# Kernel optimization log

Hardware: AMD Instinct MI355X
Metric: run time of the kernel (lower is better)

## Reference

```python
import math
import jax, jax.numpy as jnp
import numpy as np

H = 12
D = 64  # head dim

def _heads(x):
    # [b, n, h*d] -> [b, h, n, d]
    b, n, _ = x.shape
    return x.reshape(b, n, H, D).transpose(0, 2, 1, 3)

def setup_inputs() -> dict:
    key = jax.random.key(0)
    ks = jax.random.split(key, 9)
    hs = 768
    s = 1.0 / math.sqrt(hs)
    return {
        "query_states": jax.random.normal(ks[0], (8, 1024, hs), jnp.float32),
        "key_states": jax.random.normal(ks[1], (8, 1024, hs), jnp.float32),
        "Wd": jax.random.normal(ks[2], (hs, hs), jnp.float32) * s,
        "Wq": jax.random.normal(ks[3], (hs, hs), jnp.float32) * s,
        "bq": jax.random.normal(ks[4], (hs,), jnp.float32) * 0.01,
        "Wk": jax.random.normal(ks[5], (hs, hs), jnp.float32) * s,
        "bk": jax.random.normal(ks[6], (hs,), jnp.float32) * 0.01,
        "Wv": jax.random.normal(ks[7], (hs, hs), jnp.float32) * s,
        "bv": jax.random.normal(ks[8], (hs,), jnp.float32) * 0.01,
    }

def reference(query_states, key_states, Wd, Wq, bq, Wk, bk, Wv, bv):
    # projections (torch Linear: x @ W.T + b)
    qd = _heads(query_states @ Wd.T)          # [b,h,n,d]
    kd = _heads(key_states @ Wd.T)
    q = _heads(query_states @ Wq.T + bq)
    k = _heads(key_states @ Wk.T + bk)
    v = _heads(key_states @ Wv.T + bv)
    # -0.5 * cdist(qd, kd)^2 = -0.5*(|qd|^2 + |kd|^2) + qd@kd^T
    qd_sq = jnp.sum(qd * qd, axis=-1)          # [b,h,n]
    kd_sq = jnp.sum(kd * kd, axis=-1)          # [b,h,m]
    quad = (qd @ jnp.swapaxes(kd, -1, -2)
            - 0.5 * qd_sq[..., :, None]
            - 0.5 * kd_sq[..., None, :])       # [b,h,n,m]
    lin = q @ jnp.swapaxes(k, -1, -2)          # [b,h,n,m]
    scores = (quad + lin) / math.sqrt(D)
    probs = jax.nn.softmax(scores, axis=-1)
    ctx = probs @ v                            # [b,h,n,d]
    b, _, n, _ = ctx.shape
    return ctx.transpose(0, 2, 1, 3).reshape(b, n, H * D)
```

## Files before the change

kernel.cpp:

```cpp
#include <hip/hip_runtime.h>
#include <stdint.h>

typedef __attribute__((ext_vector_type(8))) short short8;
typedef __attribute__((ext_vector_type(4))) short short4v;
typedef __attribute__((ext_vector_type(4))) float f32x4;
typedef __attribute__((ext_vector_type(16))) float f32x16;
typedef __attribute__((ext_vector_type(4))) int int4v;

static __device__ __forceinline__ unsigned short f2b(float f) {
  unsigned int u = __builtin_bit_cast(unsigned int, f);
  u += 0x7fffu + ((u >> 16) & 1u);
  return (unsigned short)(u >> 16);
}
static __device__ __forceinline__ float b2f(unsigned short b) {
  unsigned int u = ((unsigned int)b) << 16;
  return __builtin_bit_cast(float, u);
}

#define GLD16(gp, lp)                                                          \
  __builtin_amdgcn_global_load_lds(                                            \
      (const __attribute__((address_space(1))) void*)(gp),                     \
      (__attribute__((address_space(3))) void*)(lp), 16, 0, 0)

#define MFMA16 __builtin_amdgcn_mfma_f32_16x16x32_bf16
#define MFMA32 __builtin_amdgcn_mfma_f32_32x32x16_bf16

#define CVTPK(dst, lo, hi)                                                     \
  asm("v_cvt_pk_bf16_f32 %0, %1, %2" : "=v"(dst) : "v"(lo), "v"(hi))
#define PLSWAP(x, y)                                                           \
  asm volatile("v_permlane32_swap_b32 %0, %1" : "+v"(x), "+v"(y))

#define QSC 0.18033688011112113f
#define C2 0.09016844005556057f

__global__ void cvtx_kernel(const float* __restrict__ q,
                            const float* __restrict__ k,
                            unsigned short* __restrict__ Xq,
                            unsigned short* __restrict__ Xk) {
  const int bx = blockIdx.x;
  const bool lo = bx < 6144;
  const float* src = lo ? q : k;
  unsigned short* dst = lo ? Xq : Xk;
  const int i = (lo ? bx : bx - 6144) * 256 + threadIdx.x;
  float4 v = reinterpret_cast<const float4*>(src)[i];
  short4v o;
  o.x = (short)f2b(v.x);
  o.y = (short)f2b(v.y);
  o.z = (short)f2b(v.z);
  o.w = (short)f2b(v.w);
  reinterpret_cast<short4v*>(dst)[i] = o;
}

__global__ void cvtw_kernel(const float* __restrict__ Wd,
                            const float* __restrict__ Wq,
                            const float* __restrict__ Wk,
                            const float* __restrict__ Wv,
                            unsigned short* __restrict__ Wcq,
                            unsigned short* __restrict__ Wck) {
  const int bx = blockIdx.x;
  const int seg = bx / 576;
  const int i = (bx - seg * 576) * 256 + threadIdx.x;
  const float* src;
  unsigned short* dst;
  switch (seg) {
    case 0: src = Wd; dst = Wcq; break;
    case 1: src = Wq; dst = Wcq + 589824; break;
    case 2: src = Wd; dst = Wck; break;
    case 3: src = Wk; dst = Wck + 589824; break;
    default: src = Wv; dst = Wck + 1179648; break;
  }
  float4 v = reinterpret_cast<const float4*>(src)[i];
  short4v o;
  o.x = (short)f2b(v.x);
  o.y = (short)f2b(v.y);
  o.z = (short)f2b(v.z);
  o.w = (short)f2b(v.w);
  reinterpret_cast<short4v*>(dst)[i] = o;
}

__global__ __launch_bounds__(512, 2) void proj_kernel(
    const unsigned short* __restrict__ Xq, const unsigned short* __restrict__ Xk,
    const unsigned short* __restrict__ Wcq, const unsigned short* __restrict__ Wck,
    const float* __restrict__ bq, const float* __restrict__ bk,
    const float* __restrict__ bv, unsigned short* __restrict__ Qc,
    unsigned short* __restrict__ Kc, unsigned short* __restrict__ Vt) {
  __shared__ __align__(16) short lds[3][2][256 * 32];
  const int by = blockIdx.y;
  const bool mode0 = (by < 6);
  const unsigned short* X = mode0 ? Xq : Xk;
  const unsigned short* W = mode0 ? Wcq : Wck;
  const int col0 = (mode0 ? by : by - 6) * 256;
  const int row0 = blockIdx.x * 256;
  const int tid = threadIdx.x;
  const int lane = tid & 63;
  const int wid = tid >> 6;
  const int wm = wid >> 2;
  const int wn = wid & 3;
  const int l15 = lane & 15, l4 = lane >> 4;
  const int RSWZ = (l4 ^ ((l15 >> 1) & 3)) << 4;

  f32x4 acc[8][4];
#pragma unroll
  for (int i = 0; i < 8; ++i)
#pragma unroll
    for (int j = 0; j < 4; ++j) acc[i][j] = (f32x4){0.f, 0.f, 0.f, 0.f};

  auto stage = [&](int bufi, int k0) {
#pragma unroll
    for (int iss = 0; iss < 2; ++iss) {
      const int c = iss * 512 + tid;
      const int r = c >> 2;
      const int sl = (c & 3) ^ ((c >> 3) & 3);
      const unsigned short* gp = X + (size_t)(row0 + r) * 768 + k0 + sl * 8;
      GLD16(gp, (char*)&lds[bufi][0][0] + (size_t)c * 16);
    }
#pragma unroll
    for (int iss = 0; iss < 2; ++iss) {
      const int c = iss * 512 + tid;
      const int r = c >> 2;
      const int sl = (c & 3) ^ ((c >> 3) & 3);
      const unsigned short* gp = W + (size_t)(col0 + r) * 768 + k0 + sl * 8;
      GLD16(gp, (char*)&lds[bufi][1][0] + (size_t)c * 16);
    }
  };

  stage(0, 0);
  stage(1, 32);

#pragma unroll 3
  for (int kt = 0; kt < 24; ++kt) {
    if (kt < 23) {
      asm volatile("s_waitcnt vmcnt(4) lgkmcnt(0)" ::: "memory");
    } else {
      asm volatile("s_waitcnt vmcnt(0) lgkmcnt(0)" ::: "memory");
    }
    __builtin_amdgcn_s_barrier();
    asm volatile("" ::: "memory");
    if (kt < 22) stage((kt + 2) % 3, (kt + 2) * 32);

    const char* Ab = (const char*)&lds[kt % 3][0][0];
    const char* Bb = (const char*)&lds[kt % 3][1][0];
    short8 a[8], b[4];
#pragma unroll
    for (int mt = 0; mt < 8; ++mt) {
      const int r = wm * 128 + mt * 16 + l15;
      a[mt] = *reinterpret_cast<const short8*>(Ab + r * 64 + RSWZ);
    }
#pragma unroll
    for (int nt = 0; nt < 4; ++nt) {
      const int r = wn * 64 + nt * 16 + l15;
      b[nt] = *reinterpret_cast<const short8*>(Bb + r * 64 + RSWZ);
    }
#pragma unroll
    for (int mt = 0; mt < 8; ++mt)
#pragma unroll
      for (int nt = 0; nt < 4; ++nt)
        acc[mt][nt] = MFMA16(a[mt], b[nt], acc[mt][nt], 0, 0, 0);
  }

  const int mat = mode0 ? (col0 >= 768 ? 1 : 0) : ((by - 6) / 3);
  const int cbase = col0 - mat * 768 + wn * 64;
  const float* barr = mode0 ? bq : (mat == 2 ? bv : bk);
  if (!mode0 && mat == 2) {
#pragma unroll
    for (int nt = 0; nt < 4; ++nt) {
      const int cc = cbase + nt * 16 + l15;
      const int hh = cc >> 6, dd = cc & 63;
      const float bias = barr[cc];
#pragma unroll
      for (int mt = 0; mt < 8; ++mt) {
        const int row = row0 + wm * 128 + mt * 16 + l4 * 4;
        const int bb = row >> 10, nn = row & 1023;
        short4v pv;
#pragma unroll
        for (int i = 0; i < 4; ++i)
          pv[i] = (short)f2b(acc[mt][nt][i] + bias);
        *reinterpret_cast<short4v*>(
            Vt + ((size_t)(bb * 12 + hh) * 64 + dd) * 1024 + nn) = pv;
      }
    }
  } else {
    const float scale = mode0 ? QSC : 1.0f;
    unsigned short* outC = mode0 ? Qc : Kc;
#pragma unroll
    for (int nt = 0; nt < 4; ++nt) {
      const int cc = cbase + nt * 16 + l15;
      const int hh = cc >> 6, dd = cc & 63;
      const float bias = (mat >= 1) ? barr[cc] : 0.f;
#pragma unroll
      for (int mt = 0; mt < 8; ++mt) {
#pragma unroll
        for (int i = 0; i < 4; ++i) {
          const int row = row0 + wm * 128 + mt * 16 + l4 * 4 + i;
          const int bb = row >> 10, nn = row & 1023;
          outC[((size_t)(bb * 12 + hh) * 1024 + nn) * 128 + mat * 64 + dd] =
              f2b((acc[mt][nt][i] + bias) * scale);
        }
      }
    }
  }
}

__global__ __launch_bounds__(256) void wv_kernel(
    const unsigned short* __restrict__ Kc, unsigned short* __restrict__ wq,
    const unsigned short* __restrict__ Vt, unsigned short* __restrict__ Vs) {
  __shared__ float wf[1024];
  const int bh = blockIdx.x;
  const int t = threadIdx.x;
  const int part = t & 3;
  const unsigned short* Kb = Kc + (size_t)bh * 1024 * 128;
#pragma unroll
  for (int it = 0; it < 16; ++it) {
    const int key = it * 64 + (t >> 2);
    const short8* p =
        reinterpret_cast<const short8*>(Kb + (size_t)key * 128 + part * 16);
    float s = 0.f;
    short8 x0 = p[0], x1 = p[1];
#pragma unroll
    for (int j = 0; j < 8; ++j) {
      const float f0 = b2f((unsigned short)x0[j]);
      const float f1 = b2f((unsigned short)x1[j]);
      s += f0 * f0 + f1 * f1;
    }
    s += __shfl_xor(s, 1);
    s += __shfl_xor(s, 2);
    if (part == 0) {
      const unsigned short wb = f2b(__builtin_amdgcn_exp2f(-s * C2));
      wf[key] = b2f(wb);
      wq[(size_t)bh * 1024 + key] = wb;
    }
  }
  __syncthreads();
  const unsigned short* Vb = Vt + (size_t)bh * 64 * 1024;
  unsigned short* Ob = Vs + (size_t)bh * 64 * 1024;
#pragma unroll
  for (int i = 0; i < 32; ++i) {
    const int e0 = (i * 256 + t) * 8;
    const int k0 = e0 & 1023;
    short8 v = *reinterpret_cast<const short8*>(Vb + e0);
#pragma unroll
    for (int j = 0; j < 8; ++j)
      v[j] = (short)f2b(b2f((unsigned short)v[j]) * wf[k0 + j]);
    *reinterpret_cast<short8*>(Ob + e0) = v;
  }
}

__global__ __launch_bounds__(256, 3) void attn_kernel(
    const unsigned short* __restrict__ Qc, const unsigned short* __restrict__ Kc,
    const unsigned short* __restrict__ Vs, const unsigned short* __restrict__ wq,
    float* __restrict__ out) {
  __shared__ __align__(16) short kbuf[2][64 * 128];
  __shared__ __align__(16) short vbuf[2][64 * 64];
  __shared__ __align__(16) short wbuf[1024];

  const int bh = blockIdx.x % 96;
  const int qb = blockIdx.x / 96;
  const int b = bh / 12, h = bh - b * 12;
  const int lane = threadIdx.x & 63;
  const int w = threadIdx.x >> 6;
  const int l31 = lane & 31, l5 = lane >> 5;

  const unsigned short* Kg = Kc + (size_t)bh * 1024 * 128;
  const unsigned short* Vg = Vs + (size_t)bh * 64 * 1024;

  auto stageK = [&](int bufi, int kb) {
#pragma unroll
    for (int i = 0; i < 4; ++i) {
      const int slot = i * 256 + threadIdx.x;
      const int row = slot >> 4;
      const int d0 = ((slot & 15) ^ (row & 15)) * 8;
      const unsigned short* gp = Kg + (size_t)(kb * 64 + row) * 128 + d0;
      GLD16(gp, (char*)(&kbuf[bufi][0]) + (i * 256 + w * 64) * 16);
    }
  };
  auto stageV = [&](int bufi, int kb) {
#pragma unroll
    for (int i = 0; i < 2; ++i) {
      const int slot = i * 256 + threadIdx.x;
      const int row = slot >> 3;
      const int k0 = ((slot & 7) ^ (row & 7)) * 8;
      const unsigned short* gp = Vg + (size_t)row * 1024 + kb * 64 + k0;
      GLD16(gp, (char*)(&vbuf[bufi][0]) + (i * 256 + w * 64) * 16);
    }
  };

  stageK(0, 0);
  stageV(0, 0);
  if (w < 2) {
    const unsigned short* gp = wq + (size_t)bh * 1024 + (w * 64 + lane) * 8;
    GLD16(gp, (char*)(&wbuf[0]) + w * 1024);
  }

  const unsigned short* Qb =
      Qc + ((size_t)bh * 1024 + qb * 128 + w * 32 + l31) * 128 + l5 * 8;
  short8 qf[8];
#pragma unroll
  for (int s = 0; s < 8; ++s)
    qf[s] = *reinterpret_cast<const short8*>(Qb + s * 16);

  f32x16 o0, o1, la;
#pragma unroll
  for (int r = 0; r < 16; ++r) {
    o0[r] = 0.f;
    o1[r] = 0.f;
    la[r] = 0.f;
  }
  float m = -1e30f;

  const int S4 = (lane & 15) << 4;
  const int S3 = (lane & 7) << 4;
  const int ko = l5 * 16;

  asm volatile("s_waitcnt vmcnt(0)" ::: "memory");
  __syncthreads();

  int buf = 0;
  for (int kb = 0; kb < 16; ++kb) {
    if (kb < 15) {
      stageK(buf ^ 1, kb + 1);
      stageV(buf ^ 1, kb + 1);
    }

    const char* kB = (const char*)(&kbuf[buf][0]) + l31 * 256;
    f32x16 s0, s1;
#pragma unroll
    for (int r = 0; r < 16; ++r) {
      s0[r] = 0.f;
      s1[r] = 0.f;
    }
#pragma unroll
    for (int s = 0; s < 8; ++s) {
      const int off = (s * 32 + ko) ^ S4;
      short8 a0 = *reinterpret_cast<const short8*>(kB + off);
      short8 a1 = *reinterpret_cast<const short8*>(kB + 8192 + off);
      s0 = MFMA32(a0, qf[s], s0, 0, 0, 0);
      s1 = MFMA32(a1, qf[s], s1, 0, 0, 0);
    }

    float mx = s0[0];
#pragma unroll
    for (int r = 1; r < 16; ++r) mx = fmaxf(mx, s0[r]);
#pragma unroll
    for (int r = 0; r < 16; ++r) mx = fmaxf(mx, s1[r]);
    mx = fmaxf(mx, __shfl_xor(mx, 32));

    if (!__all(mx <= m + 11.0f)) {
      const float mn = fmaxf(m, mx);
      const float c = __builtin_amdgcn_exp2f(m - mn);
      m = mn;
      float cr[16];
#pragma unroll
      for (int r = 0; r < 16; ++r)
        cr[r] = __shfl(c, (r & 3) + 8 * (r >> 2) + 4 * l5);
#pragma unroll
      for (int r = 0; r < 16; ++r) {
        la[r] *= cr[r];
        o0[r] *= cr[r];
        o1[r] *= cr[r];
      }
    }

#pragma unroll
    for (int r = 0; r < 16; ++r) {
      s0[r] = __builtin_amdgcn_exp2f(s0[r] - m);
      s1[r] = __builtin_amdgcn_exp2f(s1[r] - m);
    }
    unsigned int u[16];
#pragma unroll
    for (int j = 0; j < 8; ++j) {
      CVTPK(u[j], s0[2 * j], s0[2 * j + 1]);
      CVTPK(u[8 + j], s1[2 * j], s1[2 * j + 1]);
    }
    PLSWAP(u[0], u[2]);
    PLSWAP(u[1], u[3]);
    PLSWAP(u[4], u[6]);
    PLSWAP(u[5], u[7]);
    PLSWAP(u[8], u[10]);
    PLSWAP(u[9], u[11]);
    PLSWAP(u[12], u[14]);
    PLSWAP(u[13], u[15]);
    short8 pa[4];
    {
      int4v t0 = {(int)u[0], (int)u[1], (int)u[2], (int)u[3]};
      int4v t1 = {(int)u[4], (int)u[5], (int)u[6], (int)u[7]};
      int4v t2 = {(int)u[8], (int)u[9], (int)u[10], (int)u[11]};
      int4v t3 = {(int)u[12], (int)u[13], (int)u[14], (int)u[15]};
      pa[0] = __builtin_bit_cast(short8, t0);
      pa[1] = __builtin_bit_cast(short8, t1);
      pa[2] = __builtin_bit_cast(short8, t2);
      pa[3] = __builtin_bit_cast(short8, t3);
    }

    const char* vB = (const char*)(&vbuf[buf][0]) + l31 * 128;
    const char* wB = (const char*)(&wbuf[0]) + kb * 128 + ko;
#pragma unroll
    for (int kk = 0; kk < 4; ++kk) {
      const int off = (kk * 32 + ko) ^ S3;
      short8 v0 = *reinterpret_cast<const short8*>(vB + off);
      short8 v1 = *reinterpret_cast<const short8*>(vB + 4096 + off);
      short8 wf = *reinterpret_cast<const short8*>(wB + kk * 32);
      o0 = MFMA32(pa[kk], v0, o0, 0, 0, 0);
      o1 = MFMA32(pa[kk], v1, o1, 0, 0, 0);
      la = MFMA32(pa[kk], wf, la, 0, 0, 0);
    }

    asm volatile("s_waitcnt vmcnt(0)" ::: "memory");
    __syncthreads();
    buf ^= 1;
  }

  const int qbase = b * 1024 + qb * 128 + w * 32;
#pragma unroll
  for (int r = 0; r < 16; ++r) {
    const float iv = __builtin_amdgcn_rcpf(la[r]);
    const int q = qbase + (r & 3) + 8 * (r >> 2) + 4 * l5;
    float* op = out + (size_t)q * 768 + h * 64 + l31;
    op[0] = o0[r] * iv;
    op[32] = o1[r] * iv;
  }
}

extern "C" void kernel_launch(void* const* d_in, const int* in_sizes, int n_in,
                              void* d_out, int out_size, void* d_ws,
                              size_t ws_size, hipStream_t stream) {
  const float* query = (const float*)d_in[0];
  const float* key = (const float*)d_in[1];
  const float* Wd = (const float*)d_in[2];
  const float* Wq = (const float*)d_in[3];
  const float* bq = (const float*)d_in[4];
  const float* Wk = (const float*)d_in[5];
  const float* bk = (const float*)d_in[6];
  const float* Wv = (const float*)d_in[7];
  const float* bv = (const float*)d_in[8];
  float* out = (float*)d_out;

  char* p = (char*)d_ws;
  auto alloc = [&](size_t n) {
    char* r = p;
    p += (n + 255) & ~(size_t)255;
    return r;
  };
  unsigned short* Xq = (unsigned short*)alloc(8192ULL * 768 * 2);
  unsigned short* Xk = (unsigned short*)alloc(8192ULL * 768 * 2);
  unsigned short* Wcq = (unsigned short*)alloc(1536ULL * 768 * 2);
  unsigned short* Wck = (unsigned short*)alloc(2304ULL * 768 * 2);
  unsigned short* Qc = (unsigned short*)alloc(96ULL * 1024 * 128 * 2);
  unsigned short* Kc = (unsigned short*)alloc(96ULL * 1024 * 128 * 2);
  unsigned short* Vt = (unsigned short*)alloc(96ULL * 64 * 1024 * 2);
  unsigned short* wqv = (unsigned short*)alloc(96ULL * 1024 * 2);
  unsigned short* Vs = Xk;

  cvtx_kernel<<<12288, 256, 0, stream>>>(query, key, Xq, Xk);
  cvtw_kernel<<<2880, 256, 0, stream>>>(Wd, Wq, Wk, Wv, Wcq, Wck);

  proj_kernel<<<dim3(32, 15), 512, 0, stream>>>(Xq, Xk, Wcq, Wck, bq, bk, bv,
                                                Qc, Kc, Vt);

  wv_kernel<<<96, 256, 0, stream>>>(Kc, wqv, Vt, Vs);

  attn_kernel<<<768, 256, 0, stream>>>(Qc, Kc, Vs, wqv, out);
}
```

Baseline: 155.0 us.

## Merge conversion kernels, shrink projection tile, double-buffer, add MFMA priority hints

```diff
diff --git a/kernel.cpp b/kernel.cpp
--- a/kernel.cpp
+++ b/kernel.cpp
@@ -33,15 +33,37 @@
 #define QSC 0.18033688011112113f
 #define C2 0.09016844005556057f
 
-__global__ void cvtx_kernel(const float* __restrict__ q,
-                            const float* __restrict__ k,
-                            unsigned short* __restrict__ Xq,
-                            unsigned short* __restrict__ Xk) {
+__global__ void cvt_kernel(const float* __restrict__ q,
+                           const float* __restrict__ k,
+                           const float* __restrict__ Wd,
+                           const float* __restrict__ Wq,
+                           const float* __restrict__ Wk,
+                           const float* __restrict__ Wv,
+                           unsigned short* __restrict__ Xq,
+                           unsigned short* __restrict__ Xk,
+                           unsigned short* __restrict__ Wcq,
+                           unsigned short* __restrict__ Wck) {
   const int bx = blockIdx.x;
-  const bool lo = bx < 6144;
-  const float* src = lo ? q : k;
-  unsigned short* dst = lo ? Xq : Xk;
-  const int i = (lo ? bx : bx - 6144) * 256 + threadIdx.x;
+  const float* src;
+  unsigned short* dst;
+  int i;
+  if (bx < 12288) {
+    const bool lo = bx < 6144;
+    src = lo ? q : k;
+    dst = lo ? Xq : Xk;
+    i = (lo ? bx : bx - 6144) * 256 + threadIdx.x;
+  } else {
+    const int wb = bx - 12288;
+    const int seg = wb / 576;
+    i = (wb - seg * 576) * 256 + threadIdx.x;
+    switch (seg) {
+      case 0: src = Wd; dst = Wcq; break;
+      case 1: src = Wq; dst = Wcq + 589824; break;
+      case 2: src = Wd; dst = Wck; break;
+      case 3: src = Wk; dst = Wck + 589824; break;
+      default: src = Wv; dst = Wck + 1179648; break;
+    }
+  }
   float4 v = reinterpret_cast<const float4*>(src)[i];
   short4v o;
   o.x = (short)f2b(v.x);
@@ -51,46 +73,19 @@
   reinterpret_cast<short4v*>(dst)[i] = o;
 }
 
-__global__ void cvtw_kernel(const float* __restrict__ Wd,
-                            const float* __restrict__ Wq,
-                            const float* __restrict__ Wk,
-                            const float* __restrict__ Wv,
-                            unsigned short* __restrict__ Wcq,
-                            unsigned short* __restrict__ Wck) {
-  const int bx = blockIdx.x;
-  const int seg = bx / 576;
-  const int i = (bx - seg * 576) * 256 + threadIdx.x;
-  const float* src;
-  unsigned short* dst;
-  switch (seg) {
-    case 0: src = Wd; dst = Wcq; break;
-    case 1: src = Wq; dst = Wcq + 589824; break;
-    case 2: src = Wd; dst = Wck; break;
-    case 3: src = Wk; dst = Wck + 589824; break;
-    default: src = Wv; dst = Wck + 1179648; break;
-  }
-  float4 v = reinterpret_cast<const float4*>(src)[i];
-  short4v o;
-  o.x = (short)f2b(v.x);
-  o.y = (short)f2b(v.y);
-  o.z = (short)f2b(v.z);
-  o.w = (short)f2b(v.w);
-  reinterpret_cast<short4v*>(dst)[i] = o;
-}
-
-__global__ __launch_bounds__(512, 2) void proj_kernel(
+__global__ __launch_bounds__(512, 4) void proj_kernel(
     const unsigned short* __restrict__ Xq, const unsigned short* __restrict__ Xk,
     const unsigned short* __restrict__ Wcq, const unsigned short* __restrict__ Wck,
     const float* __restrict__ bq, const float* __restrict__ bk,
     const float* __restrict__ bv, unsigned short* __restrict__ Qc,
     unsigned short* __restrict__ Kc, unsigned short* __restrict__ Vt) {
-  __shared__ __align__(16) short lds[3][2][256 * 32];
+  __shared__ __align__(16) short lds[2][384 * 32];
   const int by = blockIdx.y;
   const bool mode0 = (by < 6);
   const unsigned short* X = mode0 ? Xq : Xk;
   const unsigned short* W = mode0 ? Wcq : Wck;
   const int col0 = (mode0 ? by : by - 6) * 256;
-  const int row0 = blockIdx.x * 256;
+  const int row0 = blockIdx.x * 128;
   const int tid = threadIdx.x;
   const int lane = tid & 63;
   const int wid = tid >> 6;
@@ -99,20 +94,19 @@
   const int l15 = lane & 15, l4 = lane >> 4;
   const int RSWZ = (l4 ^ ((l15 >> 1) & 3)) << 4;
 
-  f32x4 acc[8][4];
-#pragma unroll
-  for (int i = 0; i < 8; ++i)
+  f32x4 acc[4][4];
+#pragma unroll
+  for (int i = 0; i < 4; ++i)
 #pragma unroll
     for (int j = 0; j < 4; ++j) acc[i][j] = (f32x4){0.f, 0.f, 0.f, 0.f};
 
   auto stage = [&](int bufi, int k0) {
-#pragma unroll
-    for (int iss = 0; iss < 2; ++iss) {
-      const int c = iss * 512 + tid;
+    {
+      const int c = tid;
       const int r = c >> 2;
       const int sl = (c & 3) ^ ((c >> 3) & 3);
       const unsigned short* gp = X + (size_t)(row0 + r) * 768 + k0 + sl * 8;
-      GLD16(gp, (char*)&lds[bufi][0][0] + (size_t)c * 16);
+      GLD16(gp, (char*)&lds[bufi][0] + (size_t)c * 16);
     }
 #pragma unroll
     for (int iss = 0; iss < 2; ++iss) {
@@ -120,30 +114,24 @@
       const int r = c >> 2;
       const int sl = (c & 3) ^ ((c >> 3) & 3);
       const unsigned short* gp = W + (size_t)(col0 + r) * 768 + k0 + sl * 8;
-      GLD16(gp, (char*)&lds[bufi][1][0] + (size_t)c * 16);
+      GLD16(gp, (char*)&lds[bufi][0] + 8192 + (size_t)c * 16);
     }
   };
 
   stage(0, 0);
-  stage(1, 32);
-
-#pragma unroll 3
+  asm volatile("s_waitcnt vmcnt(0)" ::: "memory");
+  __builtin_amdgcn_s_barrier();
+
   for (int kt = 0; kt < 24; ++kt) {
-    if (kt < 23) {
-      asm volatile("s_waitcnt vmcnt(4) lgkmcnt(0)" ::: "memory");
-    } else {
-      asm volatile("s_waitcnt vmcnt(0) lgkmcnt(0)" ::: "memory");
-    }
-    __builtin_amdgcn_s_barrier();
-    asm volatile("" ::: "memory");
-    if (kt < 22) stage((kt + 2) % 3, (kt + 2) * 32);
-
-    const char* Ab = (const char*)&lds[kt % 3][0][0];
-    const char* Bb = (const char*)&lds[kt % 3][1][0];
-    short8 a[8], b[4];
-#pragma unroll
-    for (int mt = 0; mt < 8; ++mt) {
-      const int r = wm * 128 + mt * 16 + l15;
+    const int cb = kt & 1;
+    if (kt < 23) stage(cb ^ 1, (kt + 1) * 32);
+
+    const char* Ab = (const char*)&lds[cb][0];
+    const char* Bb = (const char*)&lds[cb][0] + 8192;
+    short8 a[4], b[4];
+#pragma unroll
+    for (int mt = 0; mt < 4; ++mt) {
+      const int r = wm * 64 + mt * 16 + l15;
       a[mt] = *reinterpret_cast<const short8*>(Ab + r * 64 + RSWZ);
     }
 #pragma unroll
@@ -151,11 +139,15 @@
       const int r = wn * 64 + nt * 16 + l15;
       b[nt] = *reinterpret_cast<const short8*>(Bb + r * 64 + RSWZ);
     }
-#pragma unroll
-    for (int mt = 0; mt < 8; ++mt)
+    __builtin_amdgcn_s_setprio(1);
+#pragma unroll
+    for (int mt = 0; mt < 4; ++mt)
 #pragma unroll
       for (int nt = 0; nt < 4; ++nt)
         acc[mt][nt] = MFMA16(a[mt], b[nt], acc[mt][nt], 0, 0, 0);
+    __builtin_amdgcn_s_setprio(0);
+    asm volatile("s_waitcnt vmcnt(0) lgkmcnt(0)" ::: "memory");
+    __builtin_amdgcn_s_barrier();
   }
 
   const int mat = mode0 ? (col0 >= 768 ? 1 : 0) : ((by - 6) / 3);
@@ -168,8 +160,8 @@
       const int hh = cc >> 6, dd = cc & 63;
       const float bias = barr[cc];
 #pragma unroll
-      for (int mt = 0; mt < 8; ++mt) {
-        const int row = row0 + wm * 128 + mt * 16 + l4 * 4;
+      for (int mt = 0; mt < 4; ++mt) {
+        const int row = row0 + wm * 64 + mt * 16 + l4 * 4;
         const int bb = row >> 10, nn = row & 1023;
         short4v pv;
 #pragma unroll
@@ -188,10 +180,10 @@
       const int hh = cc >> 6, dd = cc & 63;
       const float bias = (mat >= 1) ? barr[cc] : 0.f;
 #pragma unroll
-      for (int mt = 0; mt < 8; ++mt) {
+      for (int mt = 0; mt < 4; ++mt) {
 #pragma unroll
         for (int i = 0; i < 4; ++i) {
-          const int row = row0 + wm * 128 + mt * 16 + l4 * 4 + i;
+          const int row = row0 + wm * 64 + mt * 16 + l4 * 4 + i;
           const int bb = row >> 10, nn = row & 1023;
           outC[((size_t)(bb * 12 + hh) * 1024 + nn) * 128 + mat * 64 + dd] =
               f2b((acc[mt][nt][i] + bias) * scale);
@@ -328,6 +320,7 @@
       s0[r] = 0.f;
       s1[r] = 0.f;
     }
+    __builtin_amdgcn_s_setprio(1);
 #pragma unroll
     for (int s = 0; s < 8; ++s) {
       const int off = (s * 32 + ko) ^ S4;
@@ -336,6 +329,7 @@
       s0 = MFMA32(a0, qf[s], s0, 0, 0, 0);
       s1 = MFMA32(a1, qf[s], s1, 0, 0, 0);
     }
+    __builtin_amdgcn_s_setprio(0);
 
     float mx = s0[0];
 #pragma unroll
@@ -393,6 +387,7 @@
 
     const char* vB = (const char*)(&vbuf[buf][0]) + l31 * 128;
     const char* wB = (const char*)(&wbuf[0]) + kb * 128 + ko;
+    __builtin_amdgcn_s_setprio(1);
 #pragma unroll
     for (int kk = 0; kk < 4; ++kk) {
       const int off = (kk * 32 + ko) ^ S3;
@@ -403,6 +398,7 @@
       o1 = MFMA32(pa[kk], v1, o1, 0, 0, 0);
       la = MFMA32(pa[kk], wf, la, 0, 0, 0);
     }
+    __builtin_amdgcn_s_setprio(0);
 
     asm volatile("s_waitcnt vmcnt(0)" ::: "memory");
     __syncthreads();
@@ -450,10 +446,10 @@
   unsigned short* wqv = (unsigned short*)alloc(96ULL * 1024 * 2);
   unsigned short* Vs = Xk;
 
-  cvtx_kernel<<<12288, 256, 0, stream>>>(query, key, Xq, Xk);
-  cvtw_kernel<<<2880, 256, 0, stream>>>(Wd, Wq, Wk, Wv, Wcq, Wck);
-
-  proj_kernel<<<dim3(32, 15), 512, 0, stream>>>(Xq, Xk, Wcq, Wck, bq, bk, bv,
+  cvt_kernel<<<15168, 256, 0, stream>>>(query, key, Wd, Wq, Wk, Wv, Xq, Xk,
+                                        Wcq, Wck);
+
+  proj_kernel<<<dim3(64, 15), 512, 0, stream>>>(Xq, Xk, Wcq, Wck, bq, bk, bv,
                                                 Qc, Kc, Vt);
 
   wv_kernel<<<96, 256, 0, stream>>>(Kc, wqv, Vt, Vs);
```

Result: no change. 156.8 us (+1.2%).
